# Kernel tuning notes

Hardware: AMD Instinct MI355X
Metric: run time of the kernel (lower is better)

## Reference

```python
import math
import jax, jax.numpy as jnp
import numpy as np
from jax.scipy.special import erf

BATCH, SEQ, DIM = 2, 4096, 128
EMA_HEADS, DQK, DV = 16, 64, 256
NUM_BUCKETS, MAX_DIST = 32, 128


def _next_fast_len(n):
    # smallest 5-smooth integer >= n (matches scipy.fftpack.next_fast_len)
    while True:
        m = n
        for p in (2, 3, 5):
            while m % p == 0:
                m //= p
        if m == 1:
            return n
        n += 1


def _laplacian_attn(x):
    mu = math.sqrt(0.5)
    std = math.sqrt(0.25 * math.pi)
    return 0.5 * (1.0 + erf((x - mu) / (std * math.sqrt(2.0))))


def _rel_pos_bias(table, n, scale):
    # causal T5 relative position bias, bucket(q_pos - k_pos)
    pos = jnp.arange(n)
    rel = jnp.maximum(pos[:, None] - pos[None, :], 0)  # [n, n], >= 0
    max_exact = NUM_BUCKETS // 2
    is_small = rel < max_exact
    val_large = max_exact + (
        jnp.log(jnp.maximum(rel, 1).astype(jnp.float32) / max_exact)
        / math.log(MAX_DIST / max_exact) * (NUM_BUCKETS - max_exact)
    ).astype(jnp.int32)
    val_large = jnp.minimum(val_large, NUM_BUCKETS - 1)
    bucket = jnp.where(is_small, rel, val_large)
    return table[bucket, 0] * scale  # [n, n]


def _conv1d_fft(x, K, n):
    # x: [b, n, h, d] (fft over axis 1), K: [n, h] (fft over axis 0)
    fast_len = _next_fast_len(2 * n - 1)
    f_x = jnp.fft.rfft(x, n=fast_len, axis=1)
    f_K = jnp.fft.rfft(K, n=fast_len, axis=0)
    out = jnp.fft.irfft(f_x * jnp.conj(f_K)[None, :, :, None], fast_len, axis=1)
    out = jnp.roll(out, -1, axis=1)
    return out[:, fast_len - n:]  # [b, n, h, d]


def _forward(x, expansion, reduction, alphas, dampen, Wqk, bqk, gamma, beta,
             Wv, bv, rel_table, Wr, br, Wu, bu, Wh, Uh, bh):
    b, n, d = x.shape
    # ---- multi-headed EMA (causal -> unidirectional) via FFT conv ----
    xe = jnp.einsum('bnd,hd->bnhd', x, expansion)
    a = jax.nn.sigmoid(alphas)            # [h]
    dm = jax.nn.sigmoid(dampen)           # [h]
    powers = jnp.arange(n - 1, -1, -1, dtype=x.dtype)  # reversed powers
    K = a * ((1.0 - a) * dm) ** powers[:, None]        # [n, h]
    conv = _conv1d_fft(xe, K, n)
    ema = jnp.einsum('bnhd,hd->bnd', conv, reduction)  # [b, n, d]
    # ---- single-headed attention (chunk_size=-1 -> one chunk), v from x ----
    qk = jax.nn.silu(ema @ Wqk + bqk)     # [b, n, dqk]
    q = qk * gamma[0] + beta[0]
    k = qk * gamma[1] + beta[1]
    v = jax.nn.silu(x @ Wv + bv)          # [b, n, dv]
    scale = 1.0 / n                       # laplacian_attn_fn scaling
    sim = jnp.einsum('bid,bjd->bij', q, k) * scale
    sim = sim + _rel_pos_bias(rel_table, n, DQK ** 0.5)
    attn = _laplacian_attn(sim)
    causal_mask = jnp.triu(jnp.ones((n, n), dtype=bool), 1)
    attn = jnp.where(causal_mask, 0.0, attn)  # laplacian: zero after activation
    attn_out = jnp.einsum('bij,bjd->bid', attn, v)  # [b, n, dv]
    # ---- gating + output ----
    reset_gate = jax.nn.silu(ema @ Wr + br)         # [b, n, dv]
    update_gate = jax.nn.sigmoid(ema @ Wu + bu)     # [b, n, d]
    gated = attn_out * reset_gate
    H = jax.nn.silu(ema @ Wh + gated @ Uh + bh)     # [b, n, d]
    return update_gate * H + (1.0 - update_gate) * x


def setup_inputs() -> dict:
    key = jax.random.key(0)
    ks = jax.random.split(key, 18)
    def rn(i, shape, s=1.0):
        return jax.random.normal(ks[i], shape, dtype=jnp.float32) * s
    return dict(
        x=rn(0, (BATCH, SEQ, DIM)),
        expansion=rn(1, (EMA_HEADS, DIM), 0.2),
        reduction=rn(2, (EMA_HEADS, DIM), 0.2),
        alphas=rn(3, (EMA_HEADS,)),
        dampen=rn(4, (EMA_HEADS,)),
        Wqk=rn(5, (DIM, DQK), 0.05), bqk=rn(6, (DQK,), 0.02),
        gamma=rn(7, (2, DQK), 0.02), beta=jnp.zeros((2, DQK), jnp.float32),
        Wv=rn(8, (DIM, DV), 0.05), bv=rn(9, (DV,), 0.02),
        rel_table=rn(10, (NUM_BUCKETS, 1), 0.02),
        Wr=rn(11, (DIM, DV), 0.05), br=rn(12, (DV,), 0.02),
        Wu=rn(13, (DIM, DIM), 0.05), bu=rn(14, (DIM,), 0.02),
        Wh=rn(15, (DIM, DIM), 0.05), Uh=rn(16, (DV, DIM), 0.05),
        bh=rn(17, (DIM,), 0.02),
    )


def reference(x, expansion, reduction, alphas, dampen, Wqk, bqk, gamma, beta,
              Wv, bv, rel_table, Wr, br, Wu, bu, Wh, Uh, bh):
    return _forward(x, expansion, reduction, alphas, dampen, Wqk, bqk, gamma,
                    beta, Wv, bv, rel_table, Wr, br, Wu, bu, Wh, Uh, bh)
```

## Files before the change

### kernel.cpp

```cpp
#include <hip/hip_runtime.h>
#include <cstdint>
#include <cmath>

#define B_ 2
#define N_ 4096
#define D_ 128
#define H_ 16
#define DQK_ 64
#define DV_ 256

typedef float    f4_t  __attribute__((ext_vector_type(4)));
typedef float    f16f  __attribute__((ext_vector_type(16)));
typedef _Float16 h4_t  __attribute__((ext_vector_type(4)));
typedef _Float16 h8_t  __attribute__((ext_vector_type(8)));

__device__ __forceinline__ float sigmoidf_(float z) { return 1.f/(1.f + expf(-z)); }
__device__ __forceinline__ float siluf_(float z)    { return z/(1.f + expf(-z)); }
__device__ __forceinline__ f16f zero16() {
  f16f z;
#pragma unroll
  for (int i = 0; i < 16; ++i) z[i] = 0.f;
  return z;
}
__device__ __forceinline__ h8_t cat8_(h4_t a, h4_t b) {
  return __builtin_shufflevector(a, b, 0, 1, 2, 3, 4, 5, 6, 7);
}

__global__ void ema_phase1(const float* __restrict__ x, const float* __restrict__ expansion,
                           const float* __restrict__ alphas, const float* __restrict__ dampen,
                           float* __restrict__ F, _Float16* __restrict__ xh) {
  int bid = blockIdx.x;
  int dg = bid & 7, c = (bid >> 3) & 63, b = bid >> 9;
  int h = threadIdx.x & 15, dl = threadIdx.x >> 4;
  int d = dg*16 + dl;
  float a  = sigmoidf_(alphas[h]);
  float dm = sigmoidf_(dampen[h]);
  float q  = (1.f - a)*dm;
  float coef = a * expansion[h*D_ + d];
  __shared__ float xs[64][16];
  {
    int e = threadIdx.x;
    int t = e >> 2, seg = e & 3;
    const float* xp = x + ((size_t)b*N_ + c*64 + t)*D_ + dg*16 + seg*4;
    f4_t v = *(const f4_t*)xp;
    *(f4_t*)&xs[t][seg*4] = v;
    h4_t hv;
#pragma unroll
    for (int j = 0; j < 4; ++j) hv[j] = (_Float16)v[j];
    *(h4_t*)(xh + ((size_t)b*N_ + c*64 + t)*D_ + dg*16 + seg*4) = hv;
  }
  __syncthreads();
  float s = 0.f;
#pragma unroll
  for (int t = 0; t < 64; ++t) s = fmaf(q, s, coef*xs[t][dl]);
  F[(((size_t)b*H_ + h)*D_ + d)*64 + c] = s;
}

__global__ void ema_carry(const float* __restrict__ F, const float* __restrict__ alphas,
                          const float* __restrict__ dampen, float* __restrict__ carry) {
  int wid = blockIdx.x*4 + (threadIdx.x >> 6);
  int lane = threadIdx.x & 63;
  int h = (wid >> 7) & 15;
  float a  = sigmoidf_(alphas[h]);
  float dm = sigmoidf_(dampen[h]);
  float q  = (1.f - a)*dm;
  float qL = q;
#pragma unroll
  for (int i = 0; i < 6; ++i) qL *= qL;
  float A = qL;
  float Bv = F[(size_t)wid*64 + lane];
#pragma unroll
  for (int len = 1; len < 64; len <<= 1) {
    float Ap = __shfl_up(A, len);
    float Bp = __shfl_up(Bv, len);
    if (lane >= len) { Bv = fmaf(A, Bp, Bv); A = A*Ap; }
  }
  float Bprev = __shfl_up(Bv, 1);
  carry[(size_t)wid*64 + lane] = (lane == 0) ? 0.f : Bprev;
}

__global__ void ema_phase2(const float* __restrict__ x, const float* __restrict__ expansion,
                           const float* __restrict__ reduction,
                           const float* __restrict__ alphas, const float* __restrict__ dampen,
                           const float* __restrict__ carry, _Float16* __restrict__ emah) {
  int bid = blockIdx.x;
  int dg = bid & 7, c = (bid >> 3) & 63, b = bid >> 9;
  int h = threadIdx.x & 15, dl = threadIdx.x >> 4;
  int d = dg*16 + dl;
  float a  = sigmoidf_(alphas[h]);
  float dm = sigmoidf_(dampen[h]);
  float q  = (1.f - a)*dm;
  float coef = a * expansion[h*D_ + d];
  float red  = reduction[h*D_ + d];
  __shared__ float xs[64][16];
  {
    int e = threadIdx.x;
    int t = e >> 2, seg = e & 3;
    const float* xp = x + ((size_t)b*N_ + c*64 + t)*D_ + dg*16 + seg*4;
    *(f4_t*)&xs[t][seg*4] = *(const f4_t*)xp;
  }
  __syncthreads();
  float s = carry[(((size_t)b*H_ + h)*D_ + d)*64 + c];
  for (int t = 0; t < 64; ++t) {
    s = fmaf(q, s, coef*xs[t][dl]);
    float v = red * s;
    v += __shfl_xor(v, 1); v += __shfl_xor(v, 2);
    v += __shfl_xor(v, 4); v += __shfl_xor(v, 8);
    if (h == 0) emah[((size_t)b*N_ + c*64 + t)*D_ + d] = (_Float16)v;
  }
}

__global__ void prep_all(const float* __restrict__ Wqk, const float* __restrict__ Wv,
                         const float* __restrict__ Wr, const float* __restrict__ Wu,
                         const float* __restrict__ Wh,
                         const float* __restrict__ bqk, const float* __restrict__ bv,
                         const float* __restrict__ br, const float* __restrict__ bu,
                         const float* __restrict__ bh,
                         const float* __restrict__ Uh, const float* __restrict__ rel_table,
                         _Float16* __restrict__ Wt, float* __restrict__ bcat,
                         _Float16* __restrict__ Uht, float* __restrict__ bias2T) {
  int idx = blockIdx.x*256 + threadIdx.x;
  if (idx < 832*128) {
    int c = idx >> 7, d = idx & 127;
    const float* W; const float* bias; int ncol, cl;
    if (c < 64)       { W=Wqk; bias=bqk; ncol=64;  cl=c; }
    else if (c < 320) { W=Wv;  bias=bv;  ncol=256; cl=c-64; }
    else if (c < 576) { W=Wr;  bias=br;  ncol=256; cl=c-320; }
    else if (c < 704) { W=Wu;  bias=bu;  ncol=128; cl=c-576; }
    else              { W=Wh;  bias=bh;  ncol=128; cl=c-704; }
    Wt[idx] = (_Float16)W[d*ncol + cl];
    if (d == 0) bcat[c] = bias[cl];
  } else if (idx < 832*128 + 32768) {
    int i2 = idx - 832*128;
    int k = i2 >> 7, c = i2 & 127;
    Uht[(size_t)c*256 + k] = (_Float16)Uh[i2];
  } else if (idx < 832*128 + 32768 + 4096) {
    int r = idx - (832*128 + 32768);
    int bucket;
    if (r < 16) bucket = r;
    else {
      double v = log((double)r / 16.0) / log(8.0) * 16.0;
      bucket = 16 + (int)v;
      if (bucket > 31) bucket = 31;
    }
    bias2T[r] = (rel_table[bucket]*8.0f - 0.70710678f) * 1.1283792f;
  }
}

__global__ __launch_bounds__(256) void linear_mfma(
    const _Float16* __restrict__ emah, const _Float16* __restrict__ xh,
    const _Float16* __restrict__ Wt, const float* __restrict__ bcat,
    const float* __restrict__ gamma, const float* __restrict__ beta,
    _Float16* __restrict__ qh, _Float16* __restrict__ kh, _Float16* __restrict__ vTt,
    _Float16* __restrict__ resetbh, _Float16* __restrict__ updatebh,
    float* __restrict__ hemab) {
  int slab = blockIdx.x % 13, rt = blockIdx.x / 13;
  int tid = threadIdx.x;
  int lane = tid & 63, w = tid >> 6;
  int lr = lane & 15, lg = lane >> 4;
  int mode = (slab==0)?0:(slab<5)?1:(slab<9)?2:(slab<11)?3:4;
  const _Float16* src = (mode==1) ? xh : emah;
  __shared__ _Float16 As[64][136];
  __shared__ _Float16 Ws[64][136];
  {
    const h8_t* s8 = (const h8_t*)(src + (size_t)rt*64*D_);
#pragma unroll
    for (int i = 0; i < 4; ++i) {
      int idx = tid + i*256;
      int row = idx >> 4, seg = idx & 15;
      *(h8_t*)&As[row][seg*8] = s8[idx];
    }
    const h8_t* w8 = (const h8_t*)(Wt + (size_t)slab*64*D_);
#pragma unroll
    for (int i = 0; i < 4; ++i) {
      int idx = tid + i*256;
      int row = idx >> 4, seg = idx & 15;
      *(h8_t*)&Ws[row][seg*8] = w8[idx];
    }
  }
  __syncthreads();
  h8_t af8[4];
#pragma unroll
  for (int kk = 0; kk < 4; ++kk) af8[kk] = *(const h8_t*)&As[w*16 + lr][32*kk + 8*lg];
  int row0 = rt*64 + w*16 + lg*4;
#pragma unroll
  for (int ns = 0; ns < 4; ++ns) {
    f4_t acc = (f4_t){0.f,0.f,0.f,0.f};
#pragma unroll
    for (int kk = 0; kk < 4; ++kk) {
      h8_t bf8 = *(const h8_t*)&Ws[ns*16 + lr][32*kk + 8*lg];
      acc = __builtin_amdgcn_mfma_f32_16x16x32_f16(af8[kk], bf8, acc, 0, 0, 0);
    }
    int c = slab*64 + ns*16 + lr;
    float bias = bcat[c];
    if (mode == 0) {
      float g0 = gamma[c], g1 = gamma[64+c], be0 = beta[c], be1 = beta[64+c];
#pragma unroll
      for (int r = 0; r < 4; ++r) {
        float qk = siluf_(acc[r] + bias);
        size_t row = row0 + r;
        qh[row*DQK_ + c] = (_Float16)(qk*g0 + be0);
        kh[row*DQK_ + c] = (_Float16)(qk*g1 + be1);
      }
    } else if (mode == 1) {
      int cl = c - 64;
      int bb = row0 >> 12, rl = row0 & 4095;
      h4_t vv;
#pragma unroll
      for (int r = 0; r < 4; ++r) vv[r] = (_Float16)siluf_(acc[r] + bias);
      *(h4_t*)&vTt[(((size_t)bb*128 + (rl>>5))*256 + cl)*32 + (rl&31)] = vv;
    } else if (mode == 2) {
      int cl = c - 320;
#pragma unroll
      for (int r = 0; r < 4; ++r)
        resetbh[(size_t)(row0 + r)*DV_ + cl] = (_Float16)siluf_(acc[r] + bias);
    } else if (mode == 3) {
      int cl = c - 576;
#pragma unroll
      for (int r = 0; r < 4; ++r)
        updatebh[(size_t)(row0 + r)*D_ + cl] = (_Float16)sigmoidf_(acc[r] + bias);
    } else {
      int cl = c - 704;
#pragma unroll
      for (int r = 0; r < 4; ++r) hemab[(size_t)(row0 + r)*D_ + cl] = acc[r] + bias;
    }
  }
}

__global__ __launch_bounds__(256, 3) void attn_kernel(
    const _Float16* __restrict__ qh, const _Float16* __restrict__ kh,
    const _Float16* __restrict__ vTt, const float* __restrict__ bias2T,
    _Float16* __restrict__ attnp) {
  int bid = blockIdx.x;
  int it = 63 - (bid >> 5);
  int rem = bid & 31;
  int s = rem >> 1, b = rem & 1;
  int a = it >> 2, r = it & 3;
  int nblk = a + 1;
  if (s >= nblk) return;
  int T = 2*it + 2;
  int tlo = (s*T)/nblk, thi = ((s+1)*T)/nblk;
  int nt = thi - tlo;
  int base = it + 2*a*(a-1) + r*a;
  int slot = base + s;
  int i0 = it * 64;
  int tid = threadIdx.x;
  int lane = tid & 63, w = tid >> 6;
  int ih = w & 1;
  int dvh = w >> 1;
  bool prod = (dvh == 0);
  int lm = lane & 31, lg = lane >> 5;

  __shared__ __align__(16) char Vb[2][18432];
  __shared__ __align__(16) char Kb[2][4352];
  __shared__ __align__(16) char Pbuf[2][2304];
  __shared__ float biasW[320];

  int jmaxv = thi*32 - 1;
  int dlo = i0 - jmaxv;
  int cnt = 64 + jmaxv - tlo*32;
  for (int k = tid; k < cnt; k += 256) {
    int d = dlo + k;
    biasW[k] = d < 0 ? -1e38f : bias2T[d];
  }

  h8_t qf8[4];
  if (prod) {
    const _Float16* qp = qh + ((size_t)b*N_ + i0 + ih*32 + lm)*DQK_ + 8*lg;
#pragma unroll
    for (int kk = 0; kk < 4; ++kk) qf8[kk] = *(const h8_t*)(qp + 16*kk);
  }

  f16f accO[4];
#pragma unroll
  for (int i = 0; i < 4; ++i) accO[i] = zero16();

  const _Float16* kbase = kh + (size_t)b*N_*DQK_;
  const _Float16* vbase = vTt + (size_t)b*128*8192;
  int st = tid & 127;
  int kr = st >> 2, ks16 = st & 3;

  h8_t k8a, k8b, vr[8];
#define ISSUE_(JT) { \
  const _Float16* kp_ = kbase + (size_t)((JT)*32 + kr)*DQK_ + ks16*16; \
  k8a = *(const h8_t*)kp_; k8b = *(const h8_t*)(kp_ + 8); \
  const _Float16* vp_ = vbase + (size_t)(JT)*8192 + st*32; \
  _Pragma("unroll") for (int i = 0; i < 4; ++i) vr[i] = *(const h8_t*)(vp_ + i*8); \
  _Pragma("unroll") for (int i = 0; i < 4; ++i) vr[4+i] = *(const h8_t*)(vp_ + 4096 + i*8); }

#define COMMIT_(BI) { \
  char* kb_ = Kb[BI] + kr*136 + ks16*32; \
  *(h4_t*)kb_        = __builtin_shufflevector(k8a, k8a, 0,1,2,3); \
  *(h4_t*)(kb_ + 8)  = __builtin_shufflevector(k8a, k8a, 4,5,6,7); \
  *(h4_t*)(kb_ + 16) = __builtin_shufflevector(k8b, k8b, 0,1,2,3); \
  *(h4_t*)(kb_ + 24) = __builtin_shufflevector(k8b, k8b, 4,5,6,7); \
  char* va_ = Vb[BI] + st*72; \
  _Pragma("unroll") for (int i = 0; i < 4; ++i) { \
    *(h4_t*)(va_ + i*16)     = __builtin_shufflevector(vr[i], vr[i], 0,1,2,3); \
    *(h4_t*)(va_ + i*16 + 8) = __builtin_shufflevector(vr[i], vr[i], 4,5,6,7); } \
  char* vb2_ = Vb[BI] + (st + 128)*72; \
  _Pragma("unroll") for (int i = 0; i < 4; ++i) { \
    *(h4_t*)(vb2_ + i*16)     = __builtin_shufflevector(vr[4+i], vr[4+i], 0,1,2,3); \
    *(h4_t*)(vb2_ + i*16 + 8) = __builtin_shufflevector(vr[4+i], vr[4+i], 4,5,6,7); } }

  if (!prod) {
    ISSUE_(tlo);
    COMMIT_(0);
    if (nt > 1) ISSUE_(tlo + 1);
  }
  __syncthreads();

  const float C1 = 1.1283792f / 4096.f;
  int ibase = i0 + ih*32 + lm;
#pragma unroll 1
  for (int t = 0; t < nt; ++t) {
    if (prod) {
      const char* kb = Kb[t & 1];
      __builtin_amdgcn_s_setprio(1);
      f16f accS = zero16();
#pragma unroll
      for (int kk = 0; kk < 4; ++kk) {
        const char* ka = kb + lm*136 + 32*kk + 16*lg;
        h8_t kf8 = cat8_(*(const h4_t*)ka, *(const h4_t*)(ka + 8));
        accS = __builtin_amdgcn_mfma_f32_32x32x16_f16(kf8, qf8[kk], accS, 0, 0, 0);
      }
      __builtin_amdgcn_s_setprio(0);
      int idx0 = ibase - dlo - (tlo + t)*32 - 4*lg;
      char* pp = Pbuf[ih] + lm*72;
#pragma unroll
      for (int rr = 0; rr < 16; ++rr) {
        float tt = fmaf(accS[rr], C1, biasW[idx0 - 8*(rr>>2) - (rr&3)]);
        float e = tt*fmaf(tt*tt, -0.101797f, -2.304877f);
        float u = exp2f(e);
        float pv = __builtin_amdgcn_rcpf(1.f + u);
        int jl = (rr&3) + 8*(rr>>2) + 4*lg;
        *(_Float16*)(pp + jl*2) = (_Float16)pv;
      }
    } else {
      if (t+1 < nt) COMMIT_((t+1) & 1);
      if (t+2 < nt) ISSUE_(tlo + t + 2);
    }
    __syncthreads();
    h8_t pa8[2];
    {
      const char* pp = Pbuf[ih] + lm*72;
#pragma unroll
      for (int ks2 = 0; ks2 < 2; ++ks2) {
        const char* pa_ = pp + 32*ks2 + 16*lg;
        pa8[ks2] = cat8_(*(const h4_t*)pa_, *(const h4_t*)(pa_ + 8));
      }
    }
    const char* vb = Vb[t & 1];
    __builtin_amdgcn_s_setprio(1);
#pragma unroll
    for (int ks2 = 0; ks2 < 2; ++ks2) {
#pragma unroll
      for (int dvb = 0; dvb < 4; ++dvb) {
        const char* va = vb + (dvh*128 + dvb*32 + lm)*72 + 32*ks2 + 16*lg;
        h8_t vf8 = cat8_(*(const h4_t*)va, *(const h4_t*)(va + 8));
        accO[dvb] = __builtin_amdgcn_mfma_f32_32x32x16_f16(pa8[ks2], vf8, accO[dvb], 0, 0, 0);
      }
    }
    __builtin_amdgcn_s_setprio(0);
    __syncthreads();
  }
#undef ISSUE_
#undef COMMIT_

  _Float16* op = attnp + ((size_t)b*544 + slot)*(64*256);
#pragma unroll
  for (int dvb = 0; dvb < 4; ++dvb) {
    int col = dvh*128 + dvb*32 + lm;
#pragma unroll
    for (int rr = 0; rr < 16; ++rr) {
      int row = ih*32 + 8*(rr>>2) + 4*lg + (rr&3);
      op[(size_t)row*256 + col] = (_Float16)accO[dvb][rr];
    }
  }
}

__global__ void combine_gated(const _Float16* __restrict__ attnp,
                              const _Float16* __restrict__ resetbh,
                              _Float16* __restrict__ gatedh) {
  size_t fi = (size_t)blockIdx.x*256 + threadIdx.x;
  int c4 = (int)(fi & 63);
  int rr = (int)(fi >> 6);
  int b = rr >> 12, n = rr & 4095;
  int it = n >> 6, rowLocal = n & 63;
  int a = it >> 2, r = it & 3;
  int nblk = a + 1;
  int base = it + 2*a*(a-1) + r*a;
  const _Float16* ap = attnp + ((size_t)b*544 + base)*16384 + rowLocal*256 + c4*4;
  f4_t acc = (f4_t){0.f,0.f,0.f,0.f};
  for (int s2 = 0; s2 < nblk; ++s2) {
    h4_t pv = *(const h4_t*)(ap + (size_t)s2*16384);
#pragma unroll
    for (int j = 0; j < 4; ++j) acc[j] += (float)pv[j];
  }
  h4_t rg = *(const h4_t*)(resetbh + fi*4);
  h4_t hg;
#pragma unroll
  for (int j = 0; j < 4; ++j) hg[j] = (_Float16)(acc[j] * (float)rg[j]);
  *(h4_t*)(gatedh + fi*4) = hg;
}

__global__ __launch_bounds__(256) void final_mfma(
    const _Float16* __restrict__ gatedh, const _Float16* __restrict__ Uht,
    const float* __restrict__ hemab, const _Float16* __restrict__ updatebh,
    const float* __restrict__ x, float* __restrict__ out) {
  int rt = blockIdx.x >> 1, cs = blockIdx.x & 1;
  int tid = threadIdx.x;
  int lane = tid & 63, w = tid >> 6;
  int lr = lane & 15, lg = lane >> 4;
  int row0 = rt*64, c0 = cs*64;
  __shared__ _Float16 As[64][136];
  __shared__ _Float16 Ws[64][136];
  f4_t acc[4];
#pragma unroll
  for (int ns = 0; ns < 4; ++ns) acc[ns] = (f4_t){0.f,0.f,0.f,0.f};
#pragma unroll
  for (int kc = 0; kc < 2; ++kc) {
    __syncthreads();
#pragma unroll
    for (int i = 0; i < 4; ++i) {
      int idx = tid + i*256;
      int row = idx >> 4, seg = idx & 15;
      *(h8_t*)&As[row][seg*8] =
          *(const h8_t*)(gatedh + (size_t)(row0 + row)*DV_ + kc*128 + seg*8);
      *(h8_t*)&Ws[row][seg*8] =
          *(const h8_t*)(Uht + (size_t)(c0 + row)*DV_ + kc*128 + seg*8);
    }
    __syncthreads();
    h8_t af8[4];
#pragma unroll
    for (int kk = 0; kk < 4; ++kk) af8[kk] = *(const h8_t*)&As[w*16 + lr][32*kk + 8*lg];
#pragma unroll
    for (int ns = 0; ns < 4; ++ns) {
#pragma unroll
      for (int kk = 0; kk < 4; ++kk) {
        h8_t bf8 = *(const h8_t*)&Ws[ns*16 + lr][32*kk + 8*lg];
        acc[ns] = __builtin_amdgcn_mfma_f32_16x16x32_f16(af8[kk], bf8, acc[ns], 0, 0, 0);
      }
    }
  }
  int orow = row0 + w*16 + lg*4;
#pragma unroll
  for (int ns = 0; ns < 4; ++ns) {
    int col = c0 + ns*16 + lr;
#pragma unroll
    for (int r = 0; r < 4; ++r) {
      size_t o = (size_t)(orow + r)*D_ + col;
      float z = acc[ns][r] + hemab[o];
      float Hv = siluf_(z);
      float u  = (float)updatebh[o];
      out[o] = u*Hv + (1.f - u)*x[o];
    }
  }
}

extern "C" void kernel_launch(void* const* d_in, const int* in_sizes, int n_in,
                              void* d_out, int out_size, void* d_ws, size_t ws_size,
                              hipStream_t stream) {
  (void)in_sizes; (void)n_in; (void)out_size; (void)ws_size;
  const float* x         = (const float*)d_in[0];
  const float* expansion = (const float*)d_in[1];
  const float* reduction = (const float*)d_in[2];
  const float* alphas    = (const float*)d_in[3];
  const float* dampen    = (const float*)d_in[4];
  const float* Wqk       = (const float*)d_in[5];
  const float* bqk       = (const float*)d_in[6];
  const float* gamma     = (const float*)d_in[7];
  const float* beta      = (const float*)d_in[8];
  const float* Wv        = (const float*)d_in[9];
  const float* bv        = (const float*)d_in[10];
  const float* rel_table = (const float*)d_in[11];
  const float* Wr        = (const float*)d_in[12];
  const float* br        = (const float*)d_in[13];
  const float* Wu        = (const float*)d_in[14];
  const float* bu        = (const float*)d_in[15];
  const float* Wh        = (const float*)d_in[16];
  const float* Uh        = (const float*)d_in[17];
  const float* bh        = (const float*)d_in[18];
  float* out = (float*)d_out;

  char* p = (char*)d_ws;
  size_t off = 0;
  auto alloc = [&](size_t bytes) -> char* {
    char* r = p + off;
    off += (bytes + 255) & ~(size_t)255;
    return r;
  };
  float*    F       = (float*)alloc((size_t)B_*H_*D_*64*4);
  float*    carry   = (float*)alloc((size_t)B_*H_*D_*64*4);
  _Float16* emah    = (_Float16*)alloc((size_t)B_*N_*D_*2);
  _Float16* xh      = (_Float16*)alloc((size_t)B_*N_*D_*2);
  float*    bias2T  = (float*)alloc((size_t)N_*4);
  _Float16* Wt      = (_Float16*)alloc((size_t)832*128*2);
  float*    bcat    = (float*)alloc((size_t)832*4);
  _Float16* Uht     = (_Float16*)alloc((size_t)D_*DV_*2);
  _Float16* qh      = (_Float16*)alloc((size_t)B_*N_*DQK_*2);
  _Float16* kh      = (_Float16*)alloc((size_t)B_*N_*DQK_*2);
  _Float16* vTt     = (_Float16*)alloc((size_t)B_*DV_*N_*2);
  _Float16* resetbh = (_Float16*)alloc((size_t)B_*N_*DV_*2);
  _Float16* updatebh= (_Float16*)alloc((size_t)B_*N_*D_*2);
  float*    hemab   = (float*)alloc((size_t)B_*N_*D_*4);
  _Float16* gatedh  = (_Float16*)alloc((size_t)B_*N_*DV_*2);
  _Float16* attnp   = (_Float16*)alloc((size_t)B_*544*64*256*2);

  prep_all<<<560, 256, 0, stream>>>(Wqk, Wv, Wr, Wu, Wh, bqk, bv, br, bu, bh,
                                    Uh, rel_table, Wt, bcat, Uht, bias2T);
  ema_phase1<<<1024, 256, 0, stream>>>(x, expansion, alphas, dampen, F, xh);
  ema_carry<<<1024, 256, 0, stream>>>(F, alphas, dampen, carry);
  ema_phase2<<<1024, 256, 0, stream>>>(x, expansion, reduction, alphas, dampen, carry, emah);
  linear_mfma<<<128*13, 256, 0, stream>>>(emah, xh, Wt, bcat, gamma, beta,
                                          qh, kh, vTt, resetbh, updatebh, hemab);
  attn_kernel<<<2048, 256, 0, stream>>>(qh, kh, vTt, bias2T, attnp);
  combine_gated<<<2048, 256, 0, stream>>>(attnp, resetbh, gatedh);
  final_mfma<<<256, 256, 0, stream>>>(gatedh, Uht, hemab, updatebh, x, out);
}
```

Measured before the change: 108.2 us.

## Fuse partial-attention reduction and reset gating into final MFMA GEMM; vectorize P stores

Removes the separate combine_gated kernel and instead sums the split-KV attention partials and applies the reset gate while loading the A tile inside final_mfma. Blocks are reversed so the heaviest row tiles, which have the most partials, start first. This avoids writing and re-reading the gated intermediate and saves one launch, but the final GEMM now has only 256 blocks doing an uneven reduction, which can hurt load balance. Separately, the attention kernel now packs P values into h4 vectors before storing them to LDS instead of writing individual halves.

```diff
diff --git a/kernel.cpp b/kernel.cpp
--- a/kernel.cpp
+++ b/kernel.cpp
@@ -326,16 +326,18 @@
       }
       __builtin_amdgcn_s_setprio(0);
       int idx0 = ibase - dlo - (tlo + t)*32 - 4*lg;
-      char* pp = Pbuf[ih] + lm*72;
+      h4_t pa[4];
 #pragma unroll
       for (int rr = 0; rr < 16; ++rr) {
         float tt = fmaf(accS[rr], C1, biasW[idx0 - 8*(rr>>2) - (rr&3)]);
         float e = tt*fmaf(tt*tt, -0.101797f, -2.304877f);
         float u = exp2f(e);
         float pv = __builtin_amdgcn_rcpf(1.f + u);
-        int jl = (rr&3) + 8*(rr>>2) + 4*lg;
-        *(_Float16*)(pp + jl*2) = (_Float16)pv;
-      }
+        pa[rr>>2][rr&3] = (_Float16)pv;
+      }
+      char* pp = Pbuf[ih] + lm*72 + 8*lg;
+#pragma unroll
+      for (int k2 = 0; k2 < 4; ++k2) *(h4_t*)(pp + 16*k2) = pa[k2];
     } else {
       if (t+1 < nt) COMMIT_((t+1) & 1);
       if (t+2 < nt) ISSUE_(tlo + t + 2);
@@ -379,40 +381,22 @@
   }
 }
 
-__global__ void combine_gated(const _Float16* __restrict__ attnp,
-                              const _Float16* __restrict__ resetbh,
-                              _Float16* __restrict__ gatedh) {
-  size_t fi = (size_t)blockIdx.x*256 + threadIdx.x;
-  int c4 = (int)(fi & 63);
-  int rr = (int)(fi >> 6);
-  int b = rr >> 12, n = rr & 4095;
-  int it = n >> 6, rowLocal = n & 63;
-  int a = it >> 2, r = it & 3;
-  int nblk = a + 1;
-  int base = it + 2*a*(a-1) + r*a;
-  const _Float16* ap = attnp + ((size_t)b*544 + base)*16384 + rowLocal*256 + c4*4;
-  f4_t acc = (f4_t){0.f,0.f,0.f,0.f};
-  for (int s2 = 0; s2 < nblk; ++s2) {
-    h4_t pv = *(const h4_t*)(ap + (size_t)s2*16384);
-#pragma unroll
-    for (int j = 0; j < 4; ++j) acc[j] += (float)pv[j];
-  }
-  h4_t rg = *(const h4_t*)(resetbh + fi*4);
-  h4_t hg;
-#pragma unroll
-  for (int j = 0; j < 4; ++j) hg[j] = (_Float16)(acc[j] * (float)rg[j]);
-  *(h4_t*)(gatedh + fi*4) = hg;
-}
-
 __global__ __launch_bounds__(256) void final_mfma(
-    const _Float16* __restrict__ gatedh, const _Float16* __restrict__ Uht,
-    const float* __restrict__ hemab, const _Float16* __restrict__ updatebh,
-    const float* __restrict__ x, float* __restrict__ out) {
-  int rt = blockIdx.x >> 1, cs = blockIdx.x & 1;
+    const _Float16* __restrict__ attnp, const _Float16* __restrict__ resetbh,
+    const _Float16* __restrict__ Uht, const float* __restrict__ hemab,
+    const _Float16* __restrict__ updatebh, const float* __restrict__ x,
+    float* __restrict__ out) {
+  int rt = 127 - (blockIdx.x >> 1);
+  int cs = blockIdx.x & 1;
   int tid = threadIdx.x;
   int lane = tid & 63, w = tid >> 6;
   int lr = lane & 15, lg = lane >> 4;
   int row0 = rt*64, c0 = cs*64;
+  int b = rt >> 6, it = rt & 63;
+  int a = it >> 2, r = it & 3;
+  int nblk = a + 1;
+  int base = it + 2*a*(a-1) + r*a;
+  const _Float16* ap0 = attnp + ((size_t)b*544 + base)*16384;
   __shared__ _Float16 As[64][136];
   __shared__ _Float16 Ws[64][136];
   f4_t acc[4];
@@ -425,8 +409,21 @@
     for (int i = 0; i < 4; ++i) {
       int idx = tid + i*256;
       int row = idx >> 4, seg = idx & 15;
-      *(h8_t*)&As[row][seg*8] =
-          *(const h8_t*)(gatedh + (size_t)(row0 + row)*DV_ + kc*128 + seg*8);
+      int col = kc*128 + seg*8;
+      const _Float16* ap = ap0 + row*256 + col;
+      float s8[8];
+#pragma unroll
+      for (int j = 0; j < 8; ++j) s8[j] = 0.f;
+      for (int s2 = 0; s2 < nblk; ++s2) {
+        h8_t pv = *(const h8_t*)(ap + (size_t)s2*16384);
+#pragma unroll
+        for (int j = 0; j < 8; ++j) s8[j] += (float)pv[j];
+      }
+      h8_t rg = *(const h8_t*)(resetbh + (size_t)(row0 + row)*DV_ + col);
+      h8_t ga;
+#pragma unroll
+      for (int j = 0; j < 8; ++j) ga[j] = (_Float16)(s8[j] * (float)rg[j]);
+      *(h8_t*)&As[row][seg*8] = ga;
       *(h8_t*)&Ws[row][seg*8] =
           *(const h8_t*)(Uht + (size_t)(c0 + row)*DV_ + kc*128 + seg*8);
     }
@@ -448,9 +445,9 @@
   for (int ns = 0; ns < 4; ++ns) {
     int col = c0 + ns*16 + lr;
 #pragma unroll
-    for (int r = 0; r < 4; ++r) {
-      size_t o = (size_t)(orow + r)*D_ + col;
-      float z = acc[ns][r] + hemab[o];
+    for (int r2 = 0; r2 < 4; ++r2) {
+      size_t o = (size_t)(orow + r2)*D_ + col;
+      float z = acc[ns][r2] + hemab[o];
       float Hv = siluf_(z);
       float u  = (float)updatebh[o];
       out[o] = u*Hv + (1.f - u)*x[o];
@@ -504,7 +501,6 @@
   _Float16* resetbh = (_Float16*)alloc((size_t)B_*N_*DV_*2);
   _Float16* updatebh= (_Float16*)alloc((size_t)B_*N_*D_*2);
   float*    hemab   = (float*)alloc((size_t)B_*N_*D_*4);
-  _Float16* gatedh  = (_Float16*)alloc((size_t)B_*N_*DV_*2);
   _Float16* attnp   = (_Float16*)alloc((size_t)B_*544*64*256*2);
 
   prep_all<<<560, 256, 0, stream>>>(Wqk, Wv, Wr, Wu, Wh, bqk, bv, br, bu, bh,
@@ -515,6 +511,5 @@
   linear_mfma<<<128*13, 256, 0, stream>>>(emah, xh, Wt, bcat, gamma, beta,
                                           qh, kh, vTt, resetbh, updatebh, hemab);
   attn_kernel<<<2048, 256, 0, stream>>>(qh, kh, vTt, bias2T, attnp);
-  combine_gated<<<2048, 256, 0, stream>>>(attnp, resetbh, gatedh);
-  final_mfma<<<256, 256, 0, stream>>>(gatedh, Uht, hemab, updatebh, x, out);
-}
+  final_mfma<<<256, 256, 0, stream>>>(attnp, resetbh, Uht, hemab, updatebh, x, out);
+}
```

Result: slower. 134.1 us (+23.9%).
